# Kernel tuning notes

Hardware: AMD Instinct MI355X
Metric: run time of the kernel (lower is better)

The kernel has to match this reference:

```python
import jax, jax.numpy as jnp
import numpy as np

B, T, H, V = 16, 128, 512, 50257


def setup_inputs() -> dict:
    key = jax.random.key(0)
    ks = jax.random.split(key, 6)
    s = 0.05  # init_scale
    return {
        "tokens": jax.random.randint(ks[0], (B, T), 0, V, dtype=jnp.int32),
        "labels": jax.random.randint(ks[1], (B, T), 0, V, dtype=jnp.int32),
        "embedding": jax.random.normal(ks[2], (V, H), jnp.float32) * s,
        "W1": jax.random.normal(ks[3], (2 * H, 4 * H), jnp.float32) * s,
        "b1": jnp.zeros((4 * H,), jnp.float32),
        "W2": jax.random.normal(ks[4], (2 * H, 4 * H), jnp.float32) * s,
        "b2": jnp.zeros((4 * H,), jnp.float32),
        "softmax_w": jax.random.normal(ks[5], (H, V), jnp.float32) * s,
        "softmax_b": jnp.zeros((V,), jnp.float32),
    }


def _lstm_cell(x, h, c, W, b):
    # TF LSTMCell gate order: i, j (candidate), f, o; forget_bias = 0.0
    z = jnp.concatenate([x, h], axis=-1) @ W + b  # [B, 4H]
    i, j, f, o = jnp.split(z, 4, axis=-1)
    c_new = c * jax.nn.sigmoid(f) + jax.nn.sigmoid(i) * jnp.tanh(j)
    h_new = jnp.tanh(c_new) * jax.nn.sigmoid(o)
    return h_new, c_new


def _forward(tokens, labels, embedding, W1, b1, W2, b2, softmax_w, softmax_b):
    x = embedding[tokens]                 # [B, T, H] embedding lookup
    xs = jnp.swapaxes(x, 0, 1)            # [T, B, H] time-major for scan
    zeros = jnp.zeros((B, H), x.dtype)

    def step(carry, xt):
        c1, h1, c2, h2 = carry
        h1n, c1n = _lstm_cell(xt, h1, c1, W1, b1)
        h2n, c2n = _lstm_cell(h1n, h2, c2, W2, b2)
        return (c1n, h1n, c2n, h2n), h2n

    _, hs = jax.lax.scan(step, (zeros, zeros, zeros, zeros), xs)  # hs: [T, B, H]
    output = jnp.swapaxes(hs, 0, 1).reshape(-1, H)                # [B*T, H]
    logits = output @ softmax_w + softmax_b                       # [B*T, V]
    logp = jax.nn.log_softmax(logits, axis=-1)
    ll = jnp.take_along_axis(logp, labels.reshape(-1, 1), axis=1)[:, 0]
    cost = -jnp.sum(ll) / B  # sequence_loss_by_example summed, / batch_size
    return cost


def reference(tokens, labels, embedding, W1, b1, W2, b2, softmax_w, softmax_b):
    return _forward(tokens, labels, embedding, W1, b1, W2, b2, softmax_w, softmax_b)
```

## Files before the change

### kernel.cpp

```cpp
#include <hip/hip_runtime.h>

#define B_ 16
#define T_ 128
#define H_ 512
#define V_ 50257
#define VP_ 50304
#define NBLK 393
#define M_ (B_*T_)
#define N4H 2048
#define KH 512
#define NKB 16
#define FP_ 32
#define NTILES (NBLK * 16)
#define NPAIR (NTILES / 2)
#define NWORK 224
#define NCHUNK (VP_ * 16 / 16)
#define HP_ 520

typedef __attribute__((ext_vector_type(8))) short short8;
typedef __attribute__((ext_vector_type(4))) float floatx4;
typedef unsigned long long u64;

static __device__ __forceinline__ unsigned short f2bf(float f) {
    unsigned int u = __builtin_bit_cast(unsigned int, f);
    unsigned int r = (u + 0x7FFFu + ((u >> 16) & 1u)) >> 16;
    return (unsigned short)r;
}
static __device__ __forceinline__ void st_ic(u64* p, u64 v) {
    __hip_atomic_store(p, v, __ATOMIC_RELAXED, __HIP_MEMORY_SCOPE_AGENT);
}

__global__ void k_init(const int* __restrict__ labels, int* __restrict__ lab_r,
                       unsigned short* __restrict__ zeroh, int* __restrict__ flags) {
    int tid = blockIdx.x * blockDim.x + threadIdx.x;
    if (tid < M_) {
        int t = tid >> 4, b = tid & 15;
        lab_r[tid] = labels[b * T_ + t];
    }
    if (tid < B_ * H_) zeroh[tid] = 0;
    if (tid < 34 * FP_) flags[tid] = 0;
}

__global__ void k_embed(const int* __restrict__ tokens, const float* __restrict__ emb,
                        unsigned short* __restrict__ X) {
    int tid = blockIdx.x * blockDim.x + threadIdx.x;
    if (tid >= M_ * H_) return;
    int row = tid >> 9, col = tid & 511;
    int t = row >> 4, b = row & 15;
    int tok = tokens[b * T_ + t];
    X[tid] = f2bf(emb[(size_t)tok * H_ + col]);
}

__global__ void k_pack(const float* __restrict__ src, int ld, int nvalid, int nkb,
                       int nchunks, unsigned short* __restrict__ dst) {
    int tid = blockIdx.x * blockDim.x + threadIdx.x;
    int lane = tid & 63, chunk = tid >> 6;
    if (chunk >= nchunks) return;
    int nt = chunk / nkb, kb = chunk % nkb;
    int n = nt * 16 + (lane & 15);
    int k = kb * 32 + ((lane >> 4) << 3);
    unsigned short vals[8];
    if (n < nvalid) {
#pragma unroll
        for (int j = 0; j < 8; ++j) vals[j] = f2bf(src[(size_t)(k + j) * ld + n]);
    } else {
#pragma unroll
        for (int j = 0; j < 8; ++j) vals[j] = 0;
    }
    *(short8*)(dst + (size_t)chunk * 512 + lane * 8) = *(short8*)vals;
}

__global__ __launch_bounds__(256, 2) void k_gemm_bias(
        const unsigned short* __restrict__ A, const unsigned short* __restrict__ Bp,
        const float* __restrict__ bias, float* __restrict__ C) {
    int bn = blockIdx.x, bm = blockIdx.y;
    int tid = threadIdx.x, lane = tid & 63, w = tid >> 6;
    int wm = w >> 1, wn = w & 1;
    int l15 = lane & 15, quad = lane >> 4;
    floatx4 acc[4][4];
#pragma unroll
    for (int i = 0; i < 4; ++i)
#pragma unroll
        for (int j = 0; j < 4; ++j) acc[i][j] = (floatx4){0.f, 0.f, 0.f, 0.f};
    const unsigned short* Abase = A + (size_t)(bm * 128 + wm * 64 + l15) * KH + quad * 8;
    int ntg0 = bn * 8 + wn * 4;
#pragma unroll 4
    for (int kb = 0; kb < NKB; ++kb) {
        short8 af[4], bf[4];
#pragma unroll
        for (int mt = 0; mt < 4; ++mt) af[mt] = *(const short8*)(Abase + mt * 16 * KH + kb * 32);
#pragma unroll
        for (int nt = 0; nt < 4; ++nt)
            bf[nt] = *(const short8*)(Bp + ((size_t)(ntg0 + nt) * NKB + kb) * 512 + lane * 8);
#pragma unroll
        for (int mt = 0; mt < 4; ++mt)
#pragma unroll
            for (int nt = 0; nt < 4; ++nt)
                acc[mt][nt] = __builtin_amdgcn_mfma_f32_16x16x32_bf16(af[mt], bf[nt], acc[mt][nt], 0, 0, 0);
    }
#pragma unroll
    for (int nt = 0; nt < 4; ++nt) {
        int col = bn * 128 + wn * 64 + nt * 16 + l15;
        float bv = bias[col];
#pragma unroll
        for (int mt = 0; mt < 4; ++mt) {
            int row0 = bm * 128 + wm * 64 + mt * 16 + quad * 4;
#pragma unroll
            for (int r = 0; r < 4; ++r)
                C[(size_t)(row0 + r) * N4H + col] = acc[mt][nt][r] + bv;
        }
    }
}

__global__ __launch_bounds__(512, 2) void k_mega(
        const float* __restrict__ Zpre1, const float* __restrict__ W1,
        const float* __restrict__ W2, const float* __restrict__ b2,
        const unsigned short* __restrict__ zeroh,
        unsigned short* __restrict__ H1, unsigned short* __restrict__ H2,
        int* __restrict__ flags,
        const float* __restrict__ sw, unsigned short* __restrict__ SWP,
        const float* __restrict__ sb, const int* __restrict__ lab_r,
        float* __restrict__ pm, float* __restrict__ ps, float* __restrict__ labv) {
    const int blk = blockIdx.x, tid = threadIdx.x;
    const int lane = tid & 63, w = tid >> 6;
    const int l15 = lane & 15, quad = lane >> 4;
    __shared__ unsigned short hs1[16 * HP_];
    __shared__ unsigned short hs2[16 * HP_];
    __shared__ float zs[128 * 17];
    u64* H1u = (u64*)H1;
    u64* H2u = (u64*)H2;

    if (blk < 32) {
        const bool isL2 = blk >= 16;
        const int bj = isL2 ? blk - 16 : blk;
        const int g = w >> 1, half = w & 1;
        const int nt = g * 32 + bj * 2 + half;
        const int colg = g * 512 + bj * 32 + half * 16 + l15;

        short8 bfr[32];
        {
            unsigned short vals[8];
            if (!isL2) {
#pragma unroll
                for (int kb = 0; kb < 16; ++kb) {
#pragma unroll
                    for (int j = 0; j < 8; ++j)
                        vals[j] = f2bf(W1[(size_t)(512 + kb * 32 + quad * 8 + j) * N4H + nt * 16 + l15]);
                    bfr[kb] = *(short8*)vals;
                }
            } else {
#pragma unroll
                for (int kb = 0; kb < 32; ++kb) {
#pragma unroll
                    for (int j = 0; j < 8; ++j)
                        vals[j] = f2bf(W2[(size_t)(kb * 32 + quad * 8 + j) * N4H + nt * 16 + l15]);
                    bfr[kb] = *(short8*)vals;
                }
            }
        }
        const float b2c = isL2 ? b2[colg] : 0.f;
        float creg = 0.f;

        if (!isL2) {
            for (int s = 0; s < T_; ++s) {
                float zpre[4];
#pragma unroll
                for (int r = 0; r < 4; ++r)
                    zpre[r] = Zpre1[(size_t)(s * 16 + quad * 4 + r) * N4H + colg];
                if (w == 0 && s > 0) {
                    int* fp = flags + (lane & 15) * FP_;
                    while (true) {
                        int v = (lane < 16)
                            ? __hip_atomic_load(fp, __ATOMIC_RELAXED, __HIP_MEMORY_SCOPE_AGENT)
                            : 0x7fffffff;
                        if (__all(v >= s)) break;
                    }
                }
                __syncthreads();
                {
                    const short8* src = (const short8*)((s == 0) ? zeroh
                                           : H1 + (size_t)(s - 1) * B_ * H_);
#pragma unroll
                    for (int j = 0; j < 2; ++j) {
                        int idx = j * 512 + tid;
                        short8 v = src[idx];
                        *(short8*)(&hs1[(idx >> 6) * HP_ + (idx & 63) * 8]) = v;
                    }
                }
                __syncthreads();
                floatx4 a0 = (floatx4){0.f,0.f,0.f,0.f}, a1 = (floatx4){0.f,0.f,0.f,0.f};
#pragma unroll
                for (int kb = 0; kb < 8; ++kb) {
                    short8 af = *(const short8*)(&hs1[l15 * HP_ + kb * 32 + quad * 8]);
                    a0 = __builtin_amdgcn_mfma_f32_16x16x32_bf16(af, bfr[kb], a0, 0, 0, 0);
                }
#pragma unroll
                for (int kb = 8; kb < 16; ++kb) {
                    short8 af = *(const short8*)(&hs1[l15 * HP_ + kb * 32 + quad * 8]);
                    a1 = __builtin_amdgcn_mfma_f32_16x16x32_bf16(af, bfr[kb], a1, 0, 0, 0);
                }
                const int zcol = g * 32 + half * 16 + l15;
#pragma unroll
                for (int r = 0; r < 4; ++r)
                    zs[zcol * 17 + quad * 4 + r] = a0[r] + a1[r] + zpre[r];
                __syncthreads();
                {
                    int u = tid >> 4, b = tid & 15;
                    float zi = zs[(0 * 32 + u) * 17 + b];
                    float zj = zs[(1 * 32 + u) * 17 + b];
                    float zf = zs[(2 * 32 + u) * 17 + b];
                    float zo = zs[(3 * 32 + u) * 17 + b];
                    float si = 1.f / (1.f + __expf(-zi));
                    float sf = 1.f / (1.f + __expf(-zf));
                    float so = 1.f / (1.f + __expf(-zo));
                    float cn = creg * sf + si * tanhf(zj);
                    creg = cn;
                    int hvi = (int)f2bf(tanhf(cn) * so);
                    int lb = lane & 15;
                    unsigned int h0 = (unsigned int)__shfl(hvi, lb);
                    unsigned int h1v = (unsigned int)__shfl(hvi, lb + 16);
                    unsigned int h2v = (unsigned int)__shfl(hvi, lb + 32);
                    unsigned int h3v = (unsigned int)__shfl(hvi, lb + 48);
                    if (lane < 16) {
                        u64 v = (u64)(h0 | (h1v << 16)) | ((u64)(h2v | (h3v << 16)) << 32);
                        st_ic(H1u + (size_t)(s * 16 + lane) * 128 + bj * 8 + w, v);
                    }
                }
                __builtin_amdgcn_s_waitcnt(0x0F70);
                __syncthreads();
                if (tid == 0)
                    __hip_atomic_store(flags + blk * FP_, s + 1, __ATOMIC_RELAXED,
                                       __HIP_MEMORY_SCOPE_AGENT);
            }
        } else {
            for (int s = 0; s < T_; ++s) {
                if (w == 0 && s > 0) {
                    int* fp = flags + (16 + (lane & 15)) * FP_;
                    while (true) {
                        int v = (lane < 16)
                            ? __hip_atomic_load(fp, __ATOMIC_RELAXED, __HIP_MEMORY_SCOPE_AGENT)
                            : 0x7fffffff;
                        if (__all(v >= s)) break;
                    }
                }
                __syncthreads();
                {
                    const short8* s2 = (const short8*)((s == 0) ? zeroh
                                           : H2 + (size_t)(s - 1) * B_ * H_);
#pragma unroll
                    for (int j = 0; j < 2; ++j) {
                        int idx = j * 512 + tid;
                        short8 v = s2[idx];
                        *(short8*)(&hs2[(idx >> 6) * HP_ + (idx & 63) * 8]) = v;
                    }
                }
                __syncthreads();
                floatx4 a1 = (floatx4){0.f,0.f,0.f,0.f};
#pragma unroll
                for (int kb = 0; kb < 16; ++kb) {
                    short8 af = *(const short8*)(&hs2[l15 * HP_ + kb * 32 + quad * 8]);
                    a1 = __builtin_amdgcn_mfma_f32_16x16x32_bf16(af, bfr[16 + kb], a1, 0, 0, 0);
                }
                if (w == 0) {
                    int* fp = flags + (lane & 15) * FP_;
                    while (true) {
                        int v = (lane < 16)
                            ? __hip_atomic_load(fp, __ATOMIC_RELAXED, __HIP_MEMORY_SCOPE_AGENT)
                            : 0x7fffffff;
                        if (__all(v >= s + 1)) break;
                    }
                }
                __syncthreads();
                {
                    const short8* s1 = (const short8*)(H1 + (size_t)s * B_ * H_);
#pragma unroll
                    for (int j = 0; j < 2; ++j) {
                        int idx = j * 512 + tid;
                        short8 v = s1[idx];
                        *(short8*)(&hs1[(idx >> 6) * HP_ + (idx & 63) * 8]) = v;
                    }
                }
                __syncthreads();
                floatx4 a0 = (floatx4){0.f,0.f,0.f,0.f};
#pragma unroll
                for (int kb = 0; kb < 16; ++kb) {
                    short8 af = *(const short8*)(&hs1[l15 * HP_ + kb * 32 + quad * 8]);
                    a0 = __builtin_amdgcn_mfma_f32_16x16x32_bf16(af, bfr[kb], a0, 0, 0, 0);
                }
                const int zcol = g * 32 + half * 16 + l15;
#pragma unroll
                for (int r = 0; r < 4; ++r)
                    zs[zcol * 17 + quad * 4 + r] = a0[r] + a1[r] + b2c;
                __syncthreads();
                {
                    int u = tid >> 4, b = tid & 15;
                    float zi = zs[(0 * 32 + u) * 17 + b];
                    float zj = zs[(1 * 32 + u) * 17 + b];
                    float zf = zs[(2 * 32 + u) * 17 + b];
                    float zo = zs[(3 * 32 + u) * 17 + b];
                    float si = 1.f / (1.f + __expf(-zi));
                    float sf = 1.f / (1.f + __expf(-zf));
                    float so = 1.f / (1.f + __expf(-zo));
                    float cn = creg * sf + si * tanhf(zj);
                    creg = cn;
                    int hvi = (int)f2bf(tanhf(cn) * so);
                    int lb = lane & 15;
                    unsigned int h0 = (unsigned int)__shfl(hvi, lb);
                    unsigned int h1v = (unsigned int)__shfl(hvi, lb + 16);
                    unsigned int h2v = (unsigned int)__shfl(hvi, lb + 32);
                    unsigned int h3v = (unsigned int)__shfl(hvi, lb + 48);
                    if (lane < 16) {
                        u64 v = (u64)(h0 | (h1v << 16)) | ((u64)(h2v | (h3v << 16)) << 32);
                        st_ic(H2u + (size_t)(s * 16 + lane) * 128 + bj * 8 + w, v);
                    }
                }
                __builtin_amdgcn_s_waitcnt(0x0F70);
                __syncthreads();
                if (tid == 0)
                    __hip_atomic_store(flags + blk * FP_, s + 1, __ATOMIC_RELAXED,
                                       __HIP_MEMORY_SCOPE_AGENT);
            }
        }
    } else {
        const int wid = blk - 32;
        int* wdone = flags + 32 * FP_;
        const int grp = w >> 2;
        const int wig = w & 3;

        for (int t = 0; ; ++t) {
            int c = wid + NWORK * (8 * t + w);
            if (c >= NCHUNK) break;
            int cnt = c >> 4, ckb = c & 15;
            int n = cnt * 16 + l15;
            int kk = ckb * 32 + quad * 8;
            unsigned short vals[8];
            if (n < V_) {
#pragma unroll
                for (int j = 0; j < 8; ++j) vals[j] = f2bf(sw[(size_t)(kk + j) * V_ + n]);
            } else {
#pragma unroll
                for (int j = 0; j < 8; ++j) vals[j] = 0;
            }
            u64 v0 = (u64)vals[0] | ((u64)vals[1] << 16) | ((u64)vals[2] << 32) | ((u64)vals[3] << 48);
            u64 v1 = (u64)vals[4] | ((u64)vals[5] << 16) | ((u64)vals[6] << 32) | ((u64)vals[7] << 48);
            u64* dst = (u64*)(SWP + (size_t)c * 512 + lane * 8);
            st_ic(dst, v0);
            st_ic(dst + 1, v1);
        }
        __builtin_amdgcn_s_waitcnt(0x0F70);
        __syncthreads();
        if (tid == 0)
            __hip_atomic_fetch_add(wdone, 1, __ATOMIC_RELAXED, __HIP_MEMORY_SCOPE_AGENT);
        if (w == 0) {
            while (true) {
                int v = (lane == 0)
                    ? __hip_atomic_load(wdone, __ATOMIC_RELAXED, __HIP_MEMORY_SCOPE_AGENT)
                    : 0x7fffffff;
                if (__all(v >= NWORK)) break;
                __builtin_amdgcn_s_sleep(32);
            }
        }
        __syncthreads();

        int done_seen = 0;
        for (int p = wid; p < NPAIR; p += NWORK) {
            int t0 = 2 * p, t1 = 2 * p + 1;
            int bm0 = t0 / NBLK, bm1 = t1 / NBLK;
            int bmx = bm0 > bm1 ? bm0 : bm1;
            int tgt = bmx * 8 + 8;
            if (tgt > done_seen) {
                if (w == 0) {
                    int* fp = flags + (16 + (lane & 15)) * FP_;
                    while (true) {
                        int v = (lane < 16)
                            ? __hip_atomic_load(fp, __ATOMIC_RELAXED, __HIP_MEMORY_SCOPE_AGENT)
                            : 0x7fffffff;
                        if (__all(v >= tgt)) break;
                        __builtin_amdgcn_s_sleep(32);
                    }
                }
                __syncthreads();
                done_seen = tgt;
            }
            const int myt = grp ? t1 : t0;
            const int bm = myt / NBLK, bn = myt - bm * NBLK;
            floatx4 acc[2][8];
#pragma unroll
            for (int st = 0; st < 2; ++st)
#pragma unroll
                for (int j = 0; j < 8; ++j) acc[st][j] = (floatx4){0.f, 0.f, 0.f, 0.f};
            const short8* A0 = (const short8*)(H2 + (size_t)(bm * 128 + wig * 16 + l15) * KH) + quad;
            const short8* A1 = (const short8*)(H2 + (size_t)(bm * 128 + (wig + 4) * 16 + l15) * KH) + quad;
            int ntg0 = bn * 8;
#pragma unroll 4
            for (int kb = 0; kb < NKB; ++kb) {
                short8 af0 = A0[kb * 4];
                short8 af1 = A1[kb * 4];
#pragma unroll
                for (int nt = 0; nt < 8; ++nt) {
                    short8 bf = *(const short8*)(SWP + ((size_t)(ntg0 + nt) * NKB + kb) * 512 + lane * 8);
                    acc[0][nt] = __builtin_amdgcn_mfma_f32_16x16x32_bf16(af0, bf, acc[0][nt], 0, 0, 0);
                    acc[1][nt] = __builtin_amdgcn_mfma_f32_16x16x32_bf16(af1, bf, acc[1][nt], 0, 0, 0);
                }
            }
            float bv[8]; int colg[8]; bool valid[8];
#pragma unroll
            for (int nt = 0; nt < 8; ++nt) {
                colg[nt] = bn * 128 + nt * 16 + l15;
                valid[nt] = colg[nt] < V_;
                bv[nt] = valid[nt] ? sb[colg[nt]] : 0.f;
            }
#pragma unroll
            for (int st = 0; st < 2; ++st) {
#pragma unroll
                for (int r = 0; r < 4; ++r) {
                    float m = -3.0e38f;
#pragma unroll
                    for (int nt = 0; nt < 8; ++nt) {
                        float v = valid[nt] ? acc[st][nt][r] + bv[nt] : -3.0e38f;
                        acc[st][nt][r] = v;
                        m = fmaxf(m, v);
                    }
#pragma unroll
                    for (int d = 1; d < 16; d <<= 1) m = fmaxf(m, __shfl_xor(m, d, 16));
                    float sm = 0.f;
#pragma unroll
                    for (int nt = 0; nt < 8; ++nt)
                        if (valid[nt]) sm += __expf(acc[st][nt][r] - m);
#pragma unroll
                    for (int d = 1; d < 16; d <<= 1) sm += __shfl_xor(sm, d, 16);
                    int rowg = bm * 128 + (wig + st * 4) * 16 + quad * 4 + r;
                    int lc = lab_r[rowg];
#pragma unroll
                    for (int nt = 0; nt < 8; ++nt)
                        if (valid[nt] && colg[nt] == lc) labv[rowg] = acc[st][nt][r];
                    if (l15 == 0) {
                        pm[(size_t)rowg * NBLK + bn] = m;
                        ps[(size_t)rowg * NBLK + bn] = sm;
                    }
                }
            }
        }
    }
}

__global__ void k_rowreduce(const float* __restrict__ pm, const float* __restrict__ ps,
                            const float* __restrict__ labv, float* __restrict__ ll) {
    int row = blockIdx.x;
    int lane = threadIdx.x;
    const float* pmr = pm + (size_t)row * NBLK;
    const float* psr = ps + (size_t)row * NBLK;
    float m = -3.0e38f;
    for (int j = lane; j < NBLK; j += 64) m = fmaxf(m, pmr[j]);
#pragma unroll
    for (int d = 1; d < 64; d <<= 1) m = fmaxf(m, __shfl_xor(m, d, 64));
    float s = 0.f;
    for (int j = lane; j < NBLK; j += 64) s += psr[j] * __expf(pmr[j] - m);
#pragma unroll
    for (int d = 1; d < 64; d <<= 1) s += __shfl_xor(s, d, 64);
    if (lane == 0) ll[row] = labv[row] - m - logf(s);
}

__global__ void k_final(const float* __restrict__ ll, float* __restrict__ out) {
    int lane = threadIdx.x;
    float s = 0.f;
    for (int i = lane; i < M_; i += 64) s += ll[i];
#pragma unroll
    for (int d = 1; d < 64; d <<= 1) s += __shfl_xor(s, d, 64);
    if (lane == 0) out[0] = -s / (float)B_;
}

extern "C" void kernel_launch(void* const* d_in, const int* in_sizes, int n_in,
                              void* d_out, int out_size, void* d_ws, size_t ws_size,
                              hipStream_t stream) {
    const int* tokens = (const int*)d_in[0];
    const int* labels = (const int*)d_in[1];
    const float* emb = (const float*)d_in[2];
    const float* W1 = (const float*)d_in[3];
    const float* b1 = (const float*)d_in[4];
    const float* W2 = (const float*)d_in[5];
    const float* b2 = (const float*)d_in[6];
    const float* sw = (const float*)d_in[7];
    const float* sb = (const float*)d_in[8];
    float* out = (float*)d_out;

    char* ws = (char*)d_ws;
    size_t off = 0;
    auto alloc = [&](size_t bytes) {
        void* p = ws + off;
        off = (off + bytes + 255) & ~(size_t)255;
        return p;
    };
    unsigned short* X    = (unsigned short*)alloc((size_t)M_ * KH * 2);
    unsigned short* H1   = (unsigned short*)alloc((size_t)M_ * KH * 2);
    unsigned short* H2   = (unsigned short*)alloc((size_t)M_ * KH * 2);
    unsigned short* W1xP = (unsigned short*)alloc((size_t)N4H * KH * 2);
    unsigned short* SWP  = (unsigned short*)alloc((size_t)VP_ * KH * 2);
    float* Z     = (float*)alloc((size_t)M_ * N4H * 4);
    unsigned short* zeroh = (unsigned short*)alloc((size_t)B_ * H_ * 2);
    float* pm   = (float*)alloc((size_t)M_ * NBLK * 4);
    float* ps   = (float*)alloc((size_t)M_ * NBLK * 4);
    float* labv = (float*)alloc((size_t)M_ * 4);
    int*   lab_r = (int*)alloc((size_t)M_ * 4);
    float* ll   = (float*)alloc((size_t)M_ * 4);
    int*   flags = (int*)alloc((size_t)34 * FP_ * 4);

    k_init<<<64, 256, 0, stream>>>(labels, lab_r, zeroh, flags);
    k_embed<<<(M_ * H_) / 256, 256, 0, stream>>>(tokens, emb, X);
    k_pack<<<512, 256, 0, stream>>>(W1, N4H, N4H, 16, 2048, W1xP);

    k_gemm_bias<<<dim3(16, 16), 256, 0, stream>>>(X, W1xP, b1, Z);

    k_mega<<<256, 512, 0, stream>>>(Z, W1, W2, b2, zeroh, H1, H2, flags,
                                    sw, SWP, sb, lab_r, pm, ps, labv);

    k_rowreduce<<<M_, 64, 0, stream>>>(pm, ps, labv, ll);
    k_final<<<1, 64, 0, stream>>>(ll, out);
}
```

Baseline: 819.6 us.

## Replace per-step flag polling with sentinel-valued hidden-state data polling

The H1/H2 hidden-state buffers are pre-filled with an all-ones sentinel, and consumer blocks spin directly on the data words until no sentinel remains. This replaces the flag wait, the extra barrier and the store drain before each flag publish. Layer 2 now loads both h1 and h2 up front and runs both MFMA chains back to back. The aim is to cut per-step cross-block synchronization latency in the serial recurrence, at the cost of initializing the buffers and relying on 64-bit store atomicity, since a legitimate value equal to the sentinel would hang.

```diff
diff --git a/kernel.cpp b/kernel.cpp
--- a/kernel.cpp
+++ b/kernel.cpp
@@ -16,6 +16,8 @@
 #define NWORK 224
 #define NCHUNK (VP_ * 16 / 16)
 #define HP_ 520
+#define SENT 0xFFFFFFFFFFFFFFFFull
+#define HSLICE 2048
 
 typedef __attribute__((ext_vector_type(8))) short short8;
 typedef __attribute__((ext_vector_type(4))) float floatx4;
@@ -26,12 +28,16 @@
     unsigned int r = (u + 0x7FFFu + ((u >> 16) & 1u)) >> 16;
     return (unsigned short)r;
 }
+static __device__ __forceinline__ u64 ld_ic(const u64* p) {
+    return __hip_atomic_load(p, __ATOMIC_RELAXED, __HIP_MEMORY_SCOPE_AGENT);
+}
 static __device__ __forceinline__ void st_ic(u64* p, u64 v) {
     __hip_atomic_store(p, v, __ATOMIC_RELAXED, __HIP_MEMORY_SCOPE_AGENT);
 }
 
 __global__ void k_init(const int* __restrict__ labels, int* __restrict__ lab_r,
-                       unsigned short* __restrict__ zeroh, int* __restrict__ flags) {
+                       unsigned short* __restrict__ zeroh, int* __restrict__ flags,
+                       u64* __restrict__ H1u, u64* __restrict__ H2u) {
     int tid = blockIdx.x * blockDim.x + threadIdx.x;
     if (tid < M_) {
         int t = tid >> 4, b = tid & 15;
@@ -39,6 +45,11 @@
     }
     if (tid < B_ * H_) zeroh[tid] = 0;
     if (tid < 34 * FP_) flags[tid] = 0;
+#pragma unroll
+    for (int i = 0; i < 4; ++i) {
+        H1u[tid + i * 65536] = SENT;
+        H2u[tid + i * 65536] = SENT;
+    }
 }
 
 __global__ void k_embed(const int* __restrict__ tokens, const float* __restrict__ emb,
@@ -167,24 +178,21 @@
 #pragma unroll
                 for (int r = 0; r < 4; ++r)
                     zpre[r] = Zpre1[(size_t)(s * 16 + quad * 4 + r) * N4H + colg];
-                if (w == 0 && s > 0) {
-                    int* fp = flags + (lane & 15) * FP_;
-                    while (true) {
-                        int v = (lane < 16)
-                            ? __hip_atomic_load(fp, __ATOMIC_RELAXED, __HIP_MEMORY_SCOPE_AGENT)
-                            : 0x7fffffff;
-                        if (__all(v >= s)) break;
-                    }
-                }
-                __syncthreads();
                 {
-                    const short8* src = (const short8*)((s == 0) ? zeroh
-                                           : H1 + (size_t)(s - 1) * B_ * H_);
-#pragma unroll
-                    for (int j = 0; j < 2; ++j) {
+                    const u64* src = (s == 0) ? (const u64*)zeroh
+                                              : H1u + (size_t)(s - 1) * HSLICE;
+                    u64 v[4];
+#pragma unroll
+                    for (int j = 0; j < 4; ++j) v[j] = ld_ic(src + j * 512 + tid);
+                    while (v[0] == SENT || v[1] == SENT || v[2] == SENT || v[3] == SENT) {
+#pragma unroll
+                        for (int j = 0; j < 4; ++j)
+                            if (v[j] == SENT) v[j] = ld_ic(src + j * 512 + tid);
+                    }
+#pragma unroll
+                    for (int j = 0; j < 4; ++j) {
                         int idx = j * 512 + tid;
-                        short8 v = src[idx];
-                        *(short8*)(&hs1[(idx >> 6) * HP_ + (idx & 63) * 8]) = v;
+                        *(u64*)(&hs1[(idx >> 7) * HP_ + (idx & 127) * 4]) = v[j];
                     }
                 }
                 __syncthreads();
@@ -223,69 +231,48 @@
                     unsigned int h3v = (unsigned int)__shfl(hvi, lb + 48);
                     if (lane < 16) {
                         u64 v = (u64)(h0 | (h1v << 16)) | ((u64)(h2v | (h3v << 16)) << 32);
-                        st_ic(H1u + (size_t)(s * 16 + lane) * 128 + bj * 8 + w, v);
-                    }
-                }
-                __builtin_amdgcn_s_waitcnt(0x0F70);
-                __syncthreads();
-                if (tid == 0)
-                    __hip_atomic_store(flags + blk * FP_, s + 1, __ATOMIC_RELAXED,
-                                       __HIP_MEMORY_SCOPE_AGENT);
+                        st_ic(H1u + (size_t)s * HSLICE + lane * 128 + bj * 8 + w, v);
+                    }
+                }
             }
         } else {
             for (int s = 0; s < T_; ++s) {
-                if (w == 0 && s > 0) {
-                    int* fp = flags + (16 + (lane & 15)) * FP_;
-                    while (true) {
-                        int v = (lane < 16)
-                            ? __hip_atomic_load(fp, __ATOMIC_RELAXED, __HIP_MEMORY_SCOPE_AGENT)
-                            : 0x7fffffff;
-                        if (__all(v >= s)) break;
+                {
+                    const u64* s1 = H1u + (size_t)s * HSLICE;
+                    const u64* s2 = (s == 0) ? (const u64*)zeroh
+                                             : H2u + (size_t)(s - 1) * HSLICE;
+                    u64 v1[4], v2[4];
+#pragma unroll
+                    for (int j = 0; j < 4; ++j) {
+                        v1[j] = ld_ic(s1 + j * 512 + tid);
+                        v2[j] = ld_ic(s2 + j * 512 + tid);
+                    }
+                    while (v1[0] == SENT || v1[1] == SENT || v1[2] == SENT || v1[3] == SENT ||
+                           v2[0] == SENT || v2[1] == SENT || v2[2] == SENT || v2[3] == SENT) {
+#pragma unroll
+                        for (int j = 0; j < 4; ++j) {
+                            if (v1[j] == SENT) v1[j] = ld_ic(s1 + j * 512 + tid);
+                            if (v2[j] == SENT) v2[j] = ld_ic(s2 + j * 512 + tid);
+                        }
+                    }
+#pragma unroll
+                    for (int j = 0; j < 4; ++j) {
+                        int idx = j * 512 + tid;
+                        *(u64*)(&hs1[(idx >> 7) * HP_ + (idx & 127) * 4]) = v1[j];
+                        *(u64*)(&hs2[(idx >> 7) * HP_ + (idx & 127) * 4]) = v2[j];
                     }
                 }
                 __syncthreads();
-                {
-                    const short8* s2 = (const short8*)((s == 0) ? zeroh
-                                           : H2 + (size_t)(s - 1) * B_ * H_);
-#pragma unroll
-                    for (int j = 0; j < 2; ++j) {
-                        int idx = j * 512 + tid;
-                        short8 v = s2[idx];
-                        *(short8*)(&hs2[(idx >> 6) * HP_ + (idx & 63) * 8]) = v;
-                    }
-                }
-                __syncthreads();
-                floatx4 a1 = (floatx4){0.f,0.f,0.f,0.f};
+                floatx4 a0 = (floatx4){0.f,0.f,0.f,0.f}, a1 = (floatx4){0.f,0.f,0.f,0.f};
+#pragma unroll
+                for (int kb = 0; kb < 16; ++kb) {
+                    short8 af = *(const short8*)(&hs1[l15 * HP_ + kb * 32 + quad * 8]);
+                    a0 = __builtin_amdgcn_mfma_f32_16x16x32_bf16(af, bfr[kb], a0, 0, 0, 0);
+                }
 #pragma unroll
                 for (int kb = 0; kb < 16; ++kb) {
                     short8 af = *(const short8*)(&hs2[l15 * HP_ + kb * 32 + quad * 8]);
                     a1 = __builtin_amdgcn_mfma_f32_16x16x32_bf16(af, bfr[16 + kb], a1, 0, 0, 0);
-                }
-                if (w == 0) {
-                    int* fp = flags + (lane & 15) * FP_;
-                    while (true) {
-                        int v = (lane < 16)
-                            ? __hip_atomic_load(fp, __ATOMIC_RELAXED, __HIP_MEMORY_SCOPE_AGENT)
-                            : 0x7fffffff;
-                        if (__all(v >= s + 1)) break;
-                    }
-                }
-                __syncthreads();
-                {
-                    const short8* s1 = (const short8*)(H1 + (size_t)s * B_ * H_);
-#pragma unroll
-                    for (int j = 0; j < 2; ++j) {
-                        int idx = j * 512 + tid;
-                        short8 v = s1[idx];
-                        *(short8*)(&hs1[(idx >> 6) * HP_ + (idx & 63) * 8]) = v;
-                    }
-                }
-                __syncthreads();
-                floatx4 a0 = (floatx4){0.f,0.f,0.f,0.f};
-#pragma unroll
-                for (int kb = 0; kb < 16; ++kb) {
-                    short8 af = *(const short8*)(&hs1[l15 * HP_ + kb * 32 + quad * 8]);
-                    a0 = __builtin_amdgcn_mfma_f32_16x16x32_bf16(af, bfr[kb], a0, 0, 0, 0);
                 }
                 const int zcol = g * 32 + half * 16 + l15;
 #pragma unroll
@@ -311,13 +298,13 @@
                     unsigned int h3v = (unsigned int)__shfl(hvi, lb + 48);
                     if (lane < 16) {
                         u64 v = (u64)(h0 | (h1v << 16)) | ((u64)(h2v | (h3v << 16)) << 32);
-                        st_ic(H2u + (size_t)(s * 16 + lane) * 128 + bj * 8 + w, v);
+                        st_ic(H2u + (size_t)s * HSLICE + lane * 128 + bj * 8 + w, v);
                     }
                 }
                 __builtin_amdgcn_s_waitcnt(0x0F70);
                 __syncthreads();
                 if (tid == 0)
-                    __hip_atomic_store(flags + blk * FP_, s + 1, __ATOMIC_RELAXED,
+                    __hip_atomic_store(flags + (16 + bj) * FP_, s + 1, __ATOMIC_RELAXED,
                                        __HIP_MEMORY_SCOPE_AGENT);
             }
         }
@@ -505,7 +492,7 @@
     float* ll   = (float*)alloc((size_t)M_ * 4);
     int*   flags = (int*)alloc((size_t)34 * FP_ * 4);
 
-    k_init<<<64, 256, 0, stream>>>(labels, lab_r, zeroh, flags);
+    k_init<<<256, 256, 0, stream>>>(labels, lab_r, zeroh, flags, (u64*)H1, (u64*)H2);
     k_embed<<<(M_ * H_) / 256, 256, 0, stream>>>(tokens, emb, X);
     k_pack<<<512, 256, 0, stream>>>(W1, N4H, N4H, 16, 2048, W1xP);
 
```

Measured after the change: 823.4 us. No clear change (+0.5%).
